# Kernel tuning notes

Hardware: AMD Instinct MI355X
Metric: run time of the kernel (lower is better)

Reference implementation:

```python
import jax, jax.numpy as jnp
import numpy as np

N_NODES = 100000
N_EDGES = 1600000
D_IN = 128
HIDDEN = 64
N_CLASSES = 10
N_GRAPHS = 512


def setup_inputs() -> dict:
    key = jax.random.key(0)
    ks = jax.random.split(key, 9)
    x = jax.random.normal(ks[0], (N_NODES, D_IN), dtype=jnp.float32)
    edge_index = jax.random.randint(ks[1], (2, N_EDGES), 0, N_NODES, dtype=jnp.int32)
    batch = jnp.sort(jax.random.randint(ks[2], (N_NODES,), 0, N_GRAPHS, dtype=jnp.int32))
    # GCNConv: lin (no bias) + separate bias added after aggregation
    s1 = 1.0 / np.sqrt(D_IN)
    s2 = 1.0 / np.sqrt(HIDDEN)
    W1 = jax.random.uniform(ks[3], (D_IN, HIDDEN), jnp.float32, -s1, s1)
    b1 = jnp.zeros((HIDDEN,), jnp.float32)
    W2 = jax.random.uniform(ks[4], (HIDDEN, HIDDEN), jnp.float32, -s2, s2)
    b2 = jnp.zeros((HIDDEN,), jnp.float32)
    Wfc = jax.random.uniform(ks[5], (HIDDEN, N_CLASSES), jnp.float32, -s2, s2)
    bfc = jax.random.uniform(ks[6], (N_CLASSES,), jnp.float32, -s2, s2)
    return {"x": x, "edge_index": edge_index, "batch": batch,
            "W1": W1, "b1": b1, "W2": W2, "b2": b2, "Wfc": Wfc, "bfc": bfc}


def gcn_conv(x, src, dst, W, b, n_nodes):
    # symmetric normalization with added self-loops (PyG gcn_norm defaults)
    deg = jnp.zeros((n_nodes,), x.dtype).at[dst].add(1.0) + 1.0  # +1 self-loop
    dinv = jax.lax.rsqrt(deg)
    h = x @ W  # [N, out]
    coef = (dinv[src] * dinv[dst])[:, None]          # [E, 1]
    msg = h[src] * coef                               # [E, out]
    agg = jax.ops.segment_sum(msg, dst, num_segments=n_nodes)
    agg = agg + h * (dinv * dinv)[:, None]            # self-loop contribution
    return agg + b


def reference(x, edge_index, batch, W1, b1, W2, b2, Wfc, bfc):
    src, dst = edge_index[0], edge_index[1]
    n_nodes = x.shape[0]
    h = gcn_conv(x, src, dst, W1, b1, n_nodes)
    h = jax.nn.relu(h)
    # dropout skipped (inference, training=False)
    h = gcn_conv(h, src, dst, W2, b2, n_nodes)
    h = jax.nn.relu(h)
    # global mean pool over graphs
    sums = jax.ops.segment_sum(h, batch, num_segments=N_GRAPHS)
    cnts = jax.ops.segment_sum(jnp.ones((n_nodes,), h.dtype), batch, num_segments=N_GRAPHS)
    pooled = sums / jnp.maximum(cnts, 1.0)[:, None]   # [G, hidden]
    logits = pooled @ Wfc + bfc                        # [G, classes]
    return jax.nn.log_softmax(logits, axis=1)
```

## Files before the change

### kernel.cpp

```cpp
#include <hip/hip_runtime.h>
#include <cstdint>
#include <cstddef>

#define N_NODES   100000
#define N_EDGES   1600000
#define D_IN      128
#define HIDDEN    64
#define N_GRAPHS  512
#define N_CLASSES 10

#define NB   196
#define EB   1563
#define EB4  391
#define NBE  (NB * EB)
#define BCAP 12288
#define PSLOTS 8

typedef __attribute__((ext_vector_type(8))) short bf16x8;
typedef __attribute__((ext_vector_type(4))) float f32x4;
typedef __attribute__((ext_vector_type(2))) float f32x2;

__device__ inline float bf2f(unsigned short u) {
    return __uint_as_float(((unsigned int)u) << 16);
}
__device__ inline unsigned short f2bf(float f) {
    unsigned int x = __float_as_uint(f);
    return (unsigned short)((x + 0x7FFF + ((x >> 16) & 1)) >> 16);
}

__global__ __launch_bounds__(256)
void scan1_kernel(const int* __restrict__ in, int* __restrict__ bsum, int n) {
    __shared__ int lds[256];
    int tid = threadIdx.x;
    int base = blockIdx.x * 4096 + tid * 16;
    int s = 0;
#pragma unroll
    for (int j = 0; j < 16; j++) { int i = base + j; if (i < n) s += in[i]; }
    lds[tid] = s; __syncthreads();
    for (int off = 128; off > 0; off >>= 1) {
        if (tid < off) lds[tid] += lds[tid + off];
        __syncthreads();
    }
    if (tid == 0) bsum[blockIdx.x] = lds[0];
}

__global__ __launch_bounds__(256)
void scan2_kernel(int* __restrict__ bsum, int* __restrict__ out, int nb, int n) {
    __shared__ int lds[256];
    int tid = threadIdx.x;
    int v = (tid < nb) ? bsum[tid] : 0;
    lds[tid] = v; __syncthreads();
    for (int off = 1; off < 256; off <<= 1) {
        int t = (tid >= off) ? lds[tid - off] : 0;
        __syncthreads();
        lds[tid] += t;
        __syncthreads();
    }
    if (tid < nb) bsum[tid] = lds[tid] - v;
    if (tid == 255) out[n] = lds[255];
}

__global__ __launch_bounds__(256)
void scan3_kernel(const int* __restrict__ in, const int* __restrict__ bsum,
                  int* __restrict__ out, int n) {
    __shared__ int lds[256];
    int tid = threadIdx.x;
    int base = blockIdx.x * 4096 + tid * 16;
    int v[16]; int s = 0;
#pragma unroll
    for (int j = 0; j < 16; j++) {
        int i = base + j;
        v[j] = (i < n) ? in[i] : 0;
        s += v[j];
    }
    lds[tid] = s; __syncthreads();
    for (int off = 1; off < 256; off <<= 1) {
        int t = (tid >= off) ? lds[tid - off] : 0;
        __syncthreads();
        lds[tid] += t;
        __syncthreads();
    }
    int ex = lds[tid] - s + bsum[blockIdx.x];
#pragma unroll
    for (int j = 0; j < 16; j++) {
        int i = base + j;
        if (i < n) { out[i] = ex; ex += v[j]; }
    }
}

__global__ __launch_bounds__(256)
void fused1_kernel(const float* __restrict__ X, const float* __restrict__ W,
                   unsigned short* __restrict__ H,
                   const int* __restrict__ dst, int* __restrict__ HA) {
    const int tid = threadIdx.x;
    if (blockIdx.x & 1) {
        __shared__ int cnt[NB];
        int hb = blockIdx.x >> 1;
        for (int i = tid; i < NB; i += 256) cnt[i] = 0;
        __syncthreads();
        int base = hb * 1024 + tid;
#pragma unroll
        for (int j = 0; j < 4; j++) {
            int t = base + j * 256;
            if (t < N_EDGES) atomicAdd(&cnt[dst[t] >> 9], 1);
        }
        __syncthreads();
        for (int b = tid; b < NB; b += 256) HA[b * EB + hb] = cnt[b];
        return;
    }

    constexpr int K  = D_IN;
    constexpr int KP = K + 8;
    __shared__ unsigned short As[64 * KP];
    __shared__ unsigned short Wt[64 * KP];

    const int row0 = (blockIdx.x >> 1) * 64;

    for (int i = tid; i < K * 64; i += 256) {
        int k = i >> 6;
        int n = i & 63;
        Wt[n * KP + k] = f2bf(W[i]);
    }
    constexpr int KQ = K / 4;
    for (int i = tid; i < 64 * KQ; i += 256) {
        int r = i / KQ, k4 = i % KQ;
        int row = row0 + r;
        float4 v = make_float4(0.f, 0.f, 0.f, 0.f);
        if (row < N_NODES) v = ((const float4*)(X + (size_t)row * K))[k4];
        ushort4 o = make_ushort4(f2bf(v.x), f2bf(v.y), f2bf(v.z), f2bf(v.w));
        *(ushort4*)&As[r * KP + k4 * 4] = o;
    }
    __syncthreads();

    const int wave = tid >> 6;
    const int lane = tid & 63;
    const int lrow = lane & 15;
    const int quad = lane >> 4;
    const int m = wave * 16 + lrow;

    f32x4 acc0 = {0.f, 0.f, 0.f, 0.f};
    f32x4 acc1 = {0.f, 0.f, 0.f, 0.f};
    f32x4 acc2 = {0.f, 0.f, 0.f, 0.f};
    f32x4 acc3 = {0.f, 0.f, 0.f, 0.f};

#pragma unroll
    for (int kt = 0; kt < K / 32; kt++) {
        int k0 = kt * 32 + quad * 8;
        bf16x8 a = *(const bf16x8*)&As[m * KP + k0];
        bf16x8 b0 = *(const bf16x8*)&Wt[(0 * 16 + lrow) * KP + k0];
        bf16x8 b1 = *(const bf16x8*)&Wt[(1 * 16 + lrow) * KP + k0];
        bf16x8 b2 = *(const bf16x8*)&Wt[(2 * 16 + lrow) * KP + k0];
        bf16x8 b3 = *(const bf16x8*)&Wt[(3 * 16 + lrow) * KP + k0];
        acc0 = __builtin_amdgcn_mfma_f32_16x16x32_bf16(a, b0, acc0, 0, 0, 0);
        acc1 = __builtin_amdgcn_mfma_f32_16x16x32_bf16(a, b1, acc1, 0, 0, 0);
        acc2 = __builtin_amdgcn_mfma_f32_16x16x32_bf16(a, b2, acc2, 0, 0, 0);
        acc3 = __builtin_amdgcn_mfma_f32_16x16x32_bf16(a, b3, acc3, 0, 0, 0);
    }

    f32x4 accs[4] = {acc0, acc1, acc2, acc3};
#pragma unroll
    for (int c = 0; c < 4; c++) {
#pragma unroll
        for (int r = 0; r < 4; r++) {
            int row = row0 + wave * 16 + quad * 4 + r;
            if (row < N_NODES) H[(size_t)row * 64 + c * 16 + lrow] = f2bf(accs[c][r]);
        }
    }
}

__global__ __launch_bounds__(256)
void scatterA2_kernel(const int* __restrict__ src, const int* __restrict__ dst,
                      const int* __restrict__ posA, int2* __restrict__ edgeA) {
    __shared__ int off[NB];
    int tid = threadIdx.x, blk = blockIdx.x;
    for (int b = tid; b < NB; b += 256) off[b] = posA[b * EB + blk * 4];
    __syncthreads();
    int base = blk * 4096 + tid;
#pragma unroll
    for (int j = 0; j < 16; j++) {
        int t = base + j * 256;
        if (t < N_EDGES) {
            int d = dst[t];
            int r = atomicAdd(&off[d >> 9], 1);
            edgeA[r] = make_int2(d, src[t]);
        }
    }
}

__global__ __launch_bounds__(256)
void passB_kernel(const int* __restrict__ posA, const int2* __restrict__ edgeA,
                  int* __restrict__ noffs, float* __restrict__ dinv,
                  int* __restrict__ srcs2, unsigned short* __restrict__ hbuf) {
    __shared__ int hist[512];
    __shared__ int off[512];
    __shared__ int ps[256];
    __shared__ int srcs_l[BCAP];

    int tid = threadIdx.x, b = blockIdx.x;
    int e0 = posA[b * EB];
    int e1 = posA[(b + 1) * EB];
    int n0 = b << 9;
    int nn = min(512, N_NODES - n0);
    int len = e1 - e0;

    hist[tid] = 0; hist[tid + 256] = 0;
    __syncthreads();
    for (int i = e0 + tid; i < e1; i += 256) atomicAdd(&hist[edgeA[i].x - n0], 1);
    __syncthreads();

    for (int n = tid; n < nn; n += 256) dinv[n0 + n] = rsqrtf((float)hist[n] + 1.0f);

    int a0 = hist[2 * tid], a1 = hist[2 * tid + 1];
    ps[tid] = a0 + a1;
    __syncthreads();
    for (int d = 1; d < 256; d <<= 1) {
        int v = (tid >= d) ? ps[tid - d] : 0;
        __syncthreads();
        ps[tid] += v;
        __syncthreads();
    }
    int pre = ps[tid] - (a0 + a1);
    off[2 * tid] = pre;
    off[2 * tid + 1] = pre + a0;
    __syncthreads();

    for (int n = tid; n < nn; n += 256) noffs[n0 + n] = e0 + off[n];
    if (b == NB - 1 && tid == 0) noffs[N_NODES] = N_EDGES;
    __syncthreads();

    if (len <= BCAP) {
        for (int i = e0 + tid; i < e1; i += 256) {
            int2 e = edgeA[i];
            int r = atomicAdd(&off[e.x - n0], 1);
            srcs_l[r] = e.y;
        }
        __syncthreads();
        for (int i = tid; i < len; i += 256) srcs2[e0 + i] = srcs_l[i];
    } else {
        for (int i = e0 + tid; i < e1; i += 256) {
            int2 e = edgeA[i];
            int r = atomicAdd(&off[e.x - n0], 1);
            srcs2[e0 + r] = e.y;
        }
    }

    for (int idx = tid; idx < nn * 8; idx += 256) {
        int n  = idx >> 3;
        int c8 = (idx & 7) * 8;
        float d = rsqrtf((float)hist[n] + 1.0f);
        unsigned short* p = hbuf + (size_t)(n0 + n) * 64 + c8;
        int4 u = *(const int4*)p;
        int4 o;
        {
            unsigned int a = (unsigned int)u.x;
            unsigned short l = f2bf(__uint_as_float(a << 16) * d);
            unsigned short h = f2bf(__uint_as_float(a & 0xFFFF0000u) * d);
            o.x = (int)((unsigned int)l | ((unsigned int)h << 16));
        }
        {
            unsigned int a = (unsigned int)u.y;
            unsigned short l = f2bf(__uint_as_float(a << 16) * d);
            unsigned short h = f2bf(__uint_as_float(a & 0xFFFF0000u) * d);
            o.y = (int)((unsigned int)l | ((unsigned int)h << 16));
        }
        {
            unsigned int a = (unsigned int)u.z;
            unsigned short l = f2bf(__uint_as_float(a << 16) * d);
            unsigned short h = f2bf(__uint_as_float(a & 0xFFFF0000u) * d);
            o.z = (int)((unsigned int)l | ((unsigned int)h << 16));
        }
        {
            unsigned int a = (unsigned int)u.w;
            unsigned short l = f2bf(__uint_as_float(a << 16) * d);
            unsigned short h = f2bf(__uint_as_float(a & 0xFFFF0000u) * d);
            o.w = (int)((unsigned int)l | ((unsigned int)h << 16));
        }
        *(int4*)p = o;
    }
}

__device__ inline void upk_add(int4 u, float* acc) {
    unsigned int a = (unsigned int)u.x, b = (unsigned int)u.y;
    unsigned int d = (unsigned int)u.z, e = (unsigned int)u.w;
    acc[0] += __uint_as_float(a << 16);
    acc[1] += __uint_as_float(a & 0xFFFF0000u);
    acc[2] += __uint_as_float(b << 16);
    acc[3] += __uint_as_float(b & 0xFFFF0000u);
    acc[4] += __uint_as_float(d << 16);
    acc[5] += __uint_as_float(d & 0xFFFF0000u);
    acc[6] += __uint_as_float(e << 16);
    acc[7] += __uint_as_float(e & 0xFFFF0000u);
}

__device__ inline void upk8_add(int2 u, float* acc) {
    f32x2 p0 = __builtin_amdgcn_cvt_pk_f32_fp8(u.x, false);
    f32x2 p1 = __builtin_amdgcn_cvt_pk_f32_fp8(u.x, true);
    f32x2 p2 = __builtin_amdgcn_cvt_pk_f32_fp8(u.y, false);
    f32x2 p3 = __builtin_amdgcn_cvt_pk_f32_fp8(u.y, true);
    acc[0] += p0.x; acc[1] += p0.y;
    acc[2] += p1.x; acc[3] += p1.y;
    acc[4] += p2.x; acc[5] += p2.y;
    acc[6] += p3.x; acc[7] += p3.y;
}

__global__ __launch_bounds__(512)
void gather1_gemm2_kernel(const int* __restrict__ offs, const int* __restrict__ srcs,
                          const float* __restrict__ dinv, const unsigned short* __restrict__ h,
                          const float* __restrict__ b1v, const float* __restrict__ W2,
                          unsigned char* __restrict__ H8, int n_nodes) {
    constexpr int KP = 72;
    __shared__ unsigned short Hs[64 * KP];
    __shared__ unsigned short Wt[64 * KP];

    const int tid   = threadIdx.x;
    const int node0 = blockIdx.x * 64;

    for (int i = tid; i < 64 * 64; i += 512) {
        int k = i >> 6;
        int n = i & 63;
        Wt[n * KP + k] = f2bf(W2[i]);
    }

    const int g    = tid >> 3;
    const int node = node0 + g;
    const int cg   = (tid & 7) * 8;

    float acc[8];
#pragma unroll
    for (int j = 0; j < 8; j++) acc[j] = 0.f;
    float dn = 0.f;

    if (node < n_nodes) {
        dn = dinv[node];
        int4 us = *(const int4*)(h + (size_t)node * 64 + cg);
        upk_add(us, acc);

        int i = offs[node];
        const int i1 = offs[node + 1];
        int rem = i1 - i;
        if (rem > 0) {
            int s[8];
#pragma unroll
            for (int j = 0; j < 8; j++) s[j] = srcs[i + (j < rem ? j : rem - 1)];
            while (rem > 0) {
                int4 u8[8];
#pragma unroll
                for (int j = 0; j < 8; j++)
                    u8[j] = *(const int4*)(h + (size_t)s[j] * 64 + cg);
                const int cur  = rem < 8 ? rem : 8;
                const int ni   = i + cur;
                const int nrem = rem - cur;
                if (nrem > 0) {
#pragma unroll
                    for (int j = 0; j < 8; j++)
                        s[j] = srcs[ni + (j < nrem ? j : nrem - 1)];
                }
#pragma unroll
                for (int j = 0; j < 8; j++) { if (j < cur) upk_add(u8[j], acc); }
                i = ni; rem = nrem;
            }
        }
    }

    {
        float4 bv0 = *(const float4*)(b1v + cg);
        float4 bv1 = *(const float4*)(b1v + cg + 4);
        float r0 = fmaxf(dn * acc[0] + bv0.x, 0.f);
        float r1 = fmaxf(dn * acc[1] + bv0.y, 0.f);
        float r2 = fmaxf(dn * acc[2] + bv0.z, 0.f);
        float r3 = fmaxf(dn * acc[3] + bv0.w, 0.f);
        float r4 = fmaxf(dn * acc[4] + bv1.x, 0.f);
        float r5 = fmaxf(dn * acc[5] + bv1.y, 0.f);
        float r6 = fmaxf(dn * acc[6] + bv1.z, 0.f);
        float r7 = fmaxf(dn * acc[7] + bv1.w, 0.f);
        ushort4 p0 = make_ushort4(f2bf(r0), f2bf(r1), f2bf(r2), f2bf(r3));
        ushort4 p1 = make_ushort4(f2bf(r4), f2bf(r5), f2bf(r6), f2bf(r7));
        *(ushort4*)&Hs[g * KP + cg]     = p0;
        *(ushort4*)&Hs[g * KP + cg + 4] = p1;
    }
    __syncthreads();

    const int wave = tid >> 6;
    const int lane = tid & 63;
    const int lrow = lane & 15;
    const int quad = lane >> 4;
    const int rt = (wave & 3) * 16;
    const int ct = (wave >> 2) * 32;
    const int m = rt + lrow;

    f32x4 acc0 = {0.f, 0.f, 0.f, 0.f};
    f32x4 acc1 = {0.f, 0.f, 0.f, 0.f};
#pragma unroll
    for (int kt = 0; kt < 2; kt++) {
        int k0 = kt * 32 + quad * 8;
        bf16x8 a  = *(const bf16x8*)&Hs[m * KP + k0];
        bf16x8 w0 = *(const bf16x8*)&Wt[(ct + lrow) * KP + k0];
        bf16x8 w1 = *(const bf16x8*)&Wt[(ct + 16 + lrow) * KP + k0];
        acc0 = __builtin_amdgcn_mfma_f32_16x16x32_bf16(a, w0, acc0, 0, 0, 0);
        acc1 = __builtin_amdgcn_mfma_f32_16x16x32_bf16(a, w1, acc1, 0, 0, 0);
    }

    f32x4 accs[2] = {acc0, acc1};
#pragma unroll
    for (int r = 0; r < 4; r++) {
        int row = node0 + rt + quad * 4 + r;
        if (row < n_nodes) {
            float dv = dinv[row];
#pragma unroll
            for (int c = 0; c < 2; c++) {
                float v = accs[c][r] * dv;
                int p = __builtin_amdgcn_cvt_pk_fp8_f32(v, v, 0, false);
                H8[(size_t)row * 64 + ct + c * 16 + lrow] = (unsigned char)(p & 0xFF);
            }
        }
    }
}

__global__ __launch_bounds__(256)
void gather_fp8_pool_kernel(const int* __restrict__ offs, const int* __restrict__ srcs,
                            const float* __restrict__ dinv, const unsigned char* __restrict__ h8,
                            const float* __restrict__ b, const int* __restrict__ batch,
                            float* __restrict__ pooled, float* __restrict__ cnt,
                            int n_nodes) {
    __shared__ float pacc[PSLOTS][64];
    __shared__ float lcnt[PSLOTS];
    __shared__ int sg[2];

    int tid = threadIdx.x;
    int node0 = blockIdx.x * 32;
    int lastn = min(node0 + 31, n_nodes - 1);
    for (int i = tid; i < PSLOTS * 64; i += 256) ((float*)pacc)[i] = 0.f;
    if (tid < PSLOTS) lcnt[tid] = 0.f;
    if (tid == 0) { sg[0] = batch[min(node0, n_nodes - 1)]; sg[1] = batch[lastn]; }
    __syncthreads();
    int g0 = sg[0];
    bool single = (sg[0] == sg[1]);

    int node = node0 + (tid >> 3);
    int cg = (tid & 7) * 8;

    float r[8];
#pragma unroll
    for (int j = 0; j < 8; j++) r[j] = 0.f;

    if (node < n_nodes) {
        float dn = dinv[node];
        float acc[8];
#pragma unroll
        for (int j = 0; j < 8; j++) acc[j] = 0.f;
        {
            int2 u = *(const int2*)(h8 + (size_t)node * 64 + cg);
            upk8_add(u, acc);
        }

        int i = offs[node];
        const int i1 = offs[node + 1];
        int rem = i1 - i;
        if (rem > 0) {
            int s[8];
#pragma unroll
            for (int j = 0; j < 8; j++) s[j] = srcs[i + (j < rem ? j : rem - 1)];
            while (rem > 0) {
                int2 u8[8];
#pragma unroll
                for (int j = 0; j < 8; j++)
                    u8[j] = *(const int2*)(h8 + (size_t)s[j] * 64 + cg);
                const int cur  = rem < 8 ? rem : 8;
                const int ni   = i + cur;
                const int nrem = rem - cur;
                if (nrem > 0) {
#pragma unroll
                    for (int j = 0; j < 8; j++)
                        s[j] = srcs[ni + (j < nrem ? j : nrem - 1)];
                }
#pragma unroll
                for (int j = 0; j < 8; j++) { if (j < cur) upk8_add(u8[j], acc); }
                i = ni; rem = nrem;
            }
        }

        float4 b0 = *(const float4*)(b + cg);
        float4 b1 = *(const float4*)(b + cg + 4);
        r[0] = fmaxf(dn * acc[0] + b0.x, 0.f);
        r[1] = fmaxf(dn * acc[1] + b0.y, 0.f);
        r[2] = fmaxf(dn * acc[2] + b0.z, 0.f);
        r[3] = fmaxf(dn * acc[3] + b0.w, 0.f);
        r[4] = fmaxf(dn * acc[4] + b1.x, 0.f);
        r[5] = fmaxf(dn * acc[5] + b1.y, 0.f);
        r[6] = fmaxf(dn * acc[6] + b1.z, 0.f);
        r[7] = fmaxf(dn * acc[7] + b1.w, 0.f);
    }

    if (single) {
#pragma unroll
        for (int j = 0; j < 8; j++) {
            float v = r[j];
            v += __shfl_xor(v, 8);
            v += __shfl_xor(v, 16);
            v += __shfl_xor(v, 32);
            r[j] = v;
        }
        int wave = tid >> 6;
        int lane = tid & 63;
        if (lane < 8) {
#pragma unroll
            for (int j = 0; j < 8; j++) pacc[wave][lane * 8 + j] = r[j];
        }
        __syncthreads();
        if (tid < 64) {
            float s = pacc[0][tid] + pacc[1][tid] + pacc[2][tid] + pacc[3][tid];
            if (s != 0.f) unsafeAtomicAdd(&pooled[(size_t)g0 * 64 + tid], s);
        }
        if (tid == 0) {
            int valid = min(32, n_nodes - node0);
            unsafeAtomicAdd(&cnt[g0], (float)valid);
        }
    } else {
        if (node < n_nodes) {
            int g = batch[node];
            int slot = g - g0;
            if (slot < PSLOTS) {
#pragma unroll
                for (int j = 0; j < 8; j++) atomicAdd(&pacc[slot][cg + j], r[j]);
                if ((tid & 7) == 0) atomicAdd(&lcnt[slot], 1.f);
            } else {
#pragma unroll
                for (int j = 0; j < 8; j++) unsafeAtomicAdd(&pooled[(size_t)g * 64 + cg + j], r[j]);
                if ((tid & 7) == 0) unsafeAtomicAdd(&cnt[g], 1.f);
            }
        }
        __syncthreads();
        for (int i = tid; i < PSLOTS * 64; i += 256) {
            float v = ((float*)pacc)[i];
            if (v != 0.f) unsafeAtomicAdd(&pooled[(size_t)(g0 + (i >> 6)) * 64 + (i & 63)], v);
        }
        if (tid < PSLOTS && lcnt[tid] != 0.f) unsafeAtomicAdd(&cnt[g0 + tid], lcnt[tid]);
    }
}

__global__ __launch_bounds__(256)
void head_kernel(const float* __restrict__ pooled, const float* __restrict__ cnt,
                 const float* __restrict__ Wfc, const float* __restrict__ bfc,
                 float* __restrict__ out) {
    __shared__ float Ws[HIDDEN * N_CLASSES];
    __shared__ float bs[N_CLASSES];
    int tid = threadIdx.x;
    for (int i = tid; i < HIDDEN * N_CLASSES; i += 256) Ws[i] = Wfc[i];
    if (tid < N_CLASSES) bs[tid] = bfc[tid];
    __syncthreads();

    int g = blockIdx.x * 256 + tid;
    if (g >= N_GRAPHS) return;

    float inv = 1.f / fmaxf(cnt[g], 1.f);
    float p[HIDDEN];
#pragma unroll
    for (int k = 0; k < HIDDEN; k++) p[k] = pooled[(size_t)g * 64 + k] * inv;

    float lg[N_CLASSES];
    float m = -1e30f;
#pragma unroll
    for (int j = 0; j < N_CLASSES; j++) {
        float a = bs[j];
#pragma unroll
        for (int k = 0; k < HIDDEN; k++) a += p[k] * Ws[k * N_CLASSES + j];
        lg[j] = a;
        m = fmaxf(m, a);
    }
    float s = 0.f;
#pragma unroll
    for (int j = 0; j < N_CLASSES; j++) s += __expf(lg[j] - m);
    float lse = m + __logf(s);
#pragma unroll
    for (int j = 0; j < N_CLASSES; j++) out[(size_t)g * N_CLASSES + j] = lg[j] - lse;
}

extern "C" void kernel_launch(void* const* d_in, const int* in_sizes, int n_in,
                              void* d_out, int out_size, void* d_ws, size_t ws_size,
                              hipStream_t stream) {
    const float* x   = (const float*)d_in[0];
    const int*   ei  = (const int*)d_in[1];
    const int*   bat = (const int*)d_in[2];
    const float* W1  = (const float*)d_in[3];
    const float* b1  = (const float*)d_in[4];
    const float* W2  = (const float*)d_in[5];
    const float* b2  = (const float*)d_in[6];
    const float* Wfc = (const float*)d_in[7];
    const float* bfc = (const float*)d_in[8];
    float* out = (float*)d_out;

    const int* src = ei;
    const int* dst = ei + N_EDGES;

    char* ws = (char*)d_ws;

    const size_t OFF_H     = 0;
    const size_t OFF_SRCS2 = 12800000;
    const size_t OFF_NOFFS = 19200000;
    const size_t OFF_DINV  = 19600016;
    const size_t OFF_BUFB  = 25600000;
    const size_t OFF_EDGEA = 38400000;
    const size_t OFF_HA    = 51200000;
    const size_t OFF_POSA  = 52425392;
    const size_t OFF_BSUM  = 53650800;
    const size_t OFF_POOL  = 53651824;
    const size_t OFF_CNT   = 53782896;

    unsigned short* hbuf  = (unsigned short*)(ws + OFF_H);
    int*   srcs2  = (int*)  (ws + OFF_SRCS2);
    int*   noffs  = (int*)  (ws + OFF_NOFFS);
    float* dinv   = (float*)(ws + OFF_DINV);
    unsigned char* hbuf8 = (unsigned char*)(ws + OFF_BUFB);
    int2*  edgeA  = (int2*) (ws + OFF_EDGEA);
    int*   HA     = (int*)  (ws + OFF_HA);
    int*   posA   = (int*)  (ws + OFF_POSA);
    int*   bsum   = (int*)  (ws + OFF_BSUM);
    float* pooled = (float*)(ws + OFF_POOL);
    float* cnt    = (float*)(ws + OFF_CNT);

    const int SCAN_BLOCKS = (NBE + 4095) / 4096;
    const int GATHER_BLOCKS = (N_NODES * 8 + 255) / 256;
    const int GEMM_BLOCKS = (N_NODES + 63) / 64;

    hipMemsetAsync(pooled, 0, (size_t)(N_GRAPHS * 64 + N_GRAPHS) * sizeof(float), stream);

    fused1_kernel<<<2 * GEMM_BLOCKS, 256, 0, stream>>>(x, W1, hbuf, dst, HA);
    scan1_kernel<<<SCAN_BLOCKS, 256, 0, stream>>>(HA, bsum, NBE);
    scan2_kernel<<<1, 256, 0, stream>>>(bsum, posA, SCAN_BLOCKS, NBE);
    scan3_kernel<<<SCAN_BLOCKS, 256, 0, stream>>>(HA, bsum, posA, NBE);
    scatterA2_kernel<<<EB4, 256, 0, stream>>>(src, dst, posA, edgeA);
    passB_kernel<<<NB, 256, 0, stream>>>(posA, edgeA, noffs, dinv, srcs2, hbuf);

    gather1_gemm2_kernel<<<GEMM_BLOCKS, 512, 0, stream>>>(
        noffs, srcs2, dinv, hbuf, b1, W2, hbuf8, N_NODES);
    gather_fp8_pool_kernel<<<GATHER_BLOCKS, 256, 0, stream>>>(
        noffs, srcs2, dinv, hbuf8, b2, bat, pooled, cnt, N_NODES);

    head_kernel<<<(N_GRAPHS + 255) / 256, 256, 0, stream>>>(pooled, cnt, Wfc, bfc, out);
}
```

Baseline: 250.1 us.

## Split GEMM1 from histogram, fold dinv scaling into GEMM epilogue, pack edges

Splits the fused histogram/GEMM1 kernel into a standalone histogram kernel and moves GEMM1 after passB. That lets GEMM1 scale its output rows by dinv directly, which removes passB's separate read-modify-write pass over the H buffer. Edge records in the intermediate buffer are packed into one 32-bit word (local dst in the upper bits, src in the lower 17 bits) instead of int2, which halves that traffic. GEMM1 now loads X straight into registers without an LDS staging step. The cost is that the histogram can no longer overlap with the GEMM, and the packing assumes node ids fit in 17 bits.

```diff
diff --git a/kernel.cpp b/kernel.cpp
--- a/kernel.cpp
+++ b/kernel.cpp
@@ -89,54 +89,139 @@
 }
 
 __global__ __launch_bounds__(256)
-void fused1_kernel(const float* __restrict__ X, const float* __restrict__ W,
-                   unsigned short* __restrict__ H,
-                   const int* __restrict__ dst, int* __restrict__ HA) {
+void hist_kernel(const int* __restrict__ dst, int* __restrict__ HA) {
+    __shared__ int cnt[NB];
     const int tid = threadIdx.x;
-    if (blockIdx.x & 1) {
-        __shared__ int cnt[NB];
-        int hb = blockIdx.x >> 1;
-        for (int i = tid; i < NB; i += 256) cnt[i] = 0;
-        __syncthreads();
-        int base = hb * 1024 + tid;
-#pragma unroll
-        for (int j = 0; j < 4; j++) {
-            int t = base + j * 256;
-            if (t < N_EDGES) atomicAdd(&cnt[dst[t] >> 9], 1);
-        }
-        __syncthreads();
-        for (int b = tid; b < NB; b += 256) HA[b * EB + hb] = cnt[b];
-        return;
-    }
-
+    const int hb = blockIdx.x;
+    for (int i = tid; i < NB; i += 256) cnt[i] = 0;
+    __syncthreads();
+    int base = hb * 1024 + tid;
+#pragma unroll
+    for (int j = 0; j < 4; j++) {
+        int t = base + j * 256;
+        if (t < N_EDGES) atomicAdd(&cnt[dst[t] >> 9], 1);
+    }
+    __syncthreads();
+    for (int b = tid; b < NB; b += 256) HA[b * EB + hb] = cnt[b];
+}
+
+__global__ __launch_bounds__(256)
+void scatterA2_kernel(const int* __restrict__ src, const int* __restrict__ dst,
+                      const int* __restrict__ posA, unsigned int* __restrict__ edgeA) {
+    __shared__ int off[NB];
+    int tid = threadIdx.x, blk = blockIdx.x;
+    for (int b = tid; b < NB; b += 256) off[b] = posA[b * EB + blk * 4];
+    __syncthreads();
+    int base = blk * 4096 + tid;
+#pragma unroll
+    for (int j = 0; j < 16; j++) {
+        int t = base + j * 256;
+        if (t < N_EDGES) {
+            int d = dst[t];
+            unsigned int pk = (((unsigned int)(d & 511)) << 17) | (unsigned int)src[t];
+            int r = atomicAdd(&off[d >> 9], 1);
+            edgeA[r] = pk;
+        }
+    }
+}
+
+__global__ __launch_bounds__(256)
+void passB_kernel(const int* __restrict__ posA, const unsigned int* __restrict__ edgeA,
+                  int* __restrict__ noffs, float* __restrict__ dinv,
+                  int* __restrict__ srcs2) {
+    __shared__ int hist[512];
+    __shared__ int off[512];
+    __shared__ int ps[256];
+    __shared__ int srcs_l[BCAP];
+
+    int tid = threadIdx.x, b = blockIdx.x;
+    int e0 = posA[b * EB];
+    int e1 = posA[(b + 1) * EB];
+    int n0 = b << 9;
+    int nn = min(512, N_NODES - n0);
+    int len = e1 - e0;
+
+    hist[tid] = 0; hist[tid + 256] = 0;
+    __syncthreads();
+    for (int i = e0 + tid; i < e1; i += 256) atomicAdd(&hist[edgeA[i] >> 17], 1);
+    __syncthreads();
+
+    for (int n = tid; n < nn; n += 256) dinv[n0 + n] = rsqrtf((float)hist[n] + 1.0f);
+
+    int a0 = hist[2 * tid], a1 = hist[2 * tid + 1];
+    ps[tid] = a0 + a1;
+    __syncthreads();
+    for (int d = 1; d < 256; d <<= 1) {
+        int v = (tid >= d) ? ps[tid - d] : 0;
+        __syncthreads();
+        ps[tid] += v;
+        __syncthreads();
+    }
+    int pre = ps[tid] - (a0 + a1);
+    off[2 * tid] = pre;
+    off[2 * tid + 1] = pre + a0;
+    __syncthreads();
+
+    for (int n = tid; n < nn; n += 256) noffs[n0 + n] = e0 + off[n];
+    if (b == NB - 1 && tid == 0) noffs[N_NODES] = N_EDGES;
+    __syncthreads();
+
+    if (len <= BCAP) {
+        for (int i = e0 + tid; i < e1; i += 256) {
+            unsigned int e = edgeA[i];
+            int r = atomicAdd(&off[e >> 17], 1);
+            srcs_l[r] = (int)(e & 0x1FFFFu);
+        }
+        __syncthreads();
+        for (int i = tid; i < len; i += 256) srcs2[e0 + i] = srcs_l[i];
+    } else {
+        for (int i = e0 + tid; i < e1; i += 256) {
+            unsigned int e = edgeA[i];
+            int r = atomicAdd(&off[e >> 17], 1);
+            srcs2[e0 + r] = (int)(e & 0x1FFFFu);
+        }
+    }
+}
+
+__global__ __launch_bounds__(512)
+void gemm1_kernel(const float* __restrict__ X, const float* __restrict__ W,
+                  const float* __restrict__ dinv, unsigned short* __restrict__ H,
+                  int n_rows) {
     constexpr int K  = D_IN;
     constexpr int KP = K + 8;
-    __shared__ unsigned short As[64 * KP];
     __shared__ unsigned short Wt[64 * KP];
 
-    const int row0 = (blockIdx.x >> 1) * 64;
-
-    for (int i = tid; i < K * 64; i += 256) {
+    const int tid  = threadIdx.x;
+    const int row0 = blockIdx.x * 128;
+
+    for (int i = tid; i < K * 64; i += 512) {
         int k = i >> 6;
         int n = i & 63;
         Wt[n * KP + k] = f2bf(W[i]);
     }
-    constexpr int KQ = K / 4;
-    for (int i = tid; i < 64 * KQ; i += 256) {
-        int r = i / KQ, k4 = i % KQ;
-        int row = row0 + r;
-        float4 v = make_float4(0.f, 0.f, 0.f, 0.f);
-        if (row < N_NODES) v = ((const float4*)(X + (size_t)row * K))[k4];
-        ushort4 o = make_ushort4(f2bf(v.x), f2bf(v.y), f2bf(v.z), f2bf(v.w));
-        *(ushort4*)&As[r * KP + k4 * 4] = o;
-    }
-    __syncthreads();
 
     const int wave = tid >> 6;
     const int lane = tid & 63;
     const int lrow = lane & 15;
     const int quad = lane >> 4;
     const int m = wave * 16 + lrow;
+    const int row = row0 + m;
+    const bool valid = row < n_rows;
+
+    float4 xa[8];
+    if (valid) {
+        const float4* xr4 = (const float4*)(X + (size_t)row * K);
+#pragma unroll
+        for (int kt = 0; kt < 4; kt++) {
+            int q = (kt * 32 + quad * 8) >> 2;
+            xa[2 * kt]     = xr4[q];
+            xa[2 * kt + 1] = xr4[q + 1];
+        }
+    } else {
+#pragma unroll
+        for (int j = 0; j < 8; j++) xa[j] = make_float4(0.f, 0.f, 0.f, 0.f);
+    }
+    __syncthreads();
 
     f32x4 acc0 = {0.f, 0.f, 0.f, 0.f};
     f32x4 acc1 = {0.f, 0.f, 0.f, 0.f};
@@ -144,9 +229,12 @@
     f32x4 acc3 = {0.f, 0.f, 0.f, 0.f};
 
 #pragma unroll
-    for (int kt = 0; kt < K / 32; kt++) {
+    for (int kt = 0; kt < 4; kt++) {
         int k0 = kt * 32 + quad * 8;
-        bf16x8 a = *(const bf16x8*)&As[m * KP + k0];
+        const float* f = (const float*)&xa[2 * kt];
+        bf16x8 a;
+#pragma unroll
+        for (int j = 0; j < 8; j++) a[j] = (short)f2bf(f[j]);
         bf16x8 b0 = *(const bf16x8*)&Wt[(0 * 16 + lrow) * KP + k0];
         bf16x8 b1 = *(const bf16x8*)&Wt[(1 * 16 + lrow) * KP + k0];
         bf16x8 b2 = *(const bf16x8*)&Wt[(2 * 16 + lrow) * KP + k0];
@@ -159,123 +247,14 @@
 
     f32x4 accs[4] = {acc0, acc1, acc2, acc3};
 #pragma unroll
-    for (int c = 0; c < 4; c++) {
-#pragma unroll
-        for (int r = 0; r < 4; r++) {
-            int row = row0 + wave * 16 + quad * 4 + r;
-            if (row < N_NODES) H[(size_t)row * 64 + c * 16 + lrow] = f2bf(accs[c][r]);
-        }
-    }
-}
-
-__global__ __launch_bounds__(256)
-void scatterA2_kernel(const int* __restrict__ src, const int* __restrict__ dst,
-                      const int* __restrict__ posA, int2* __restrict__ edgeA) {
-    __shared__ int off[NB];
-    int tid = threadIdx.x, blk = blockIdx.x;
-    for (int b = tid; b < NB; b += 256) off[b] = posA[b * EB + blk * 4];
-    __syncthreads();
-    int base = blk * 4096 + tid;
-#pragma unroll
-    for (int j = 0; j < 16; j++) {
-        int t = base + j * 256;
-        if (t < N_EDGES) {
-            int d = dst[t];
-            int r = atomicAdd(&off[d >> 9], 1);
-            edgeA[r] = make_int2(d, src[t]);
-        }
-    }
-}
-
-__global__ __launch_bounds__(256)
-void passB_kernel(const int* __restrict__ posA, const int2* __restrict__ edgeA,
-                  int* __restrict__ noffs, float* __restrict__ dinv,
-                  int* __restrict__ srcs2, unsigned short* __restrict__ hbuf) {
-    __shared__ int hist[512];
-    __shared__ int off[512];
-    __shared__ int ps[256];
-    __shared__ int srcs_l[BCAP];
-
-    int tid = threadIdx.x, b = blockIdx.x;
-    int e0 = posA[b * EB];
-    int e1 = posA[(b + 1) * EB];
-    int n0 = b << 9;
-    int nn = min(512, N_NODES - n0);
-    int len = e1 - e0;
-
-    hist[tid] = 0; hist[tid + 256] = 0;
-    __syncthreads();
-    for (int i = e0 + tid; i < e1; i += 256) atomicAdd(&hist[edgeA[i].x - n0], 1);
-    __syncthreads();
-
-    for (int n = tid; n < nn; n += 256) dinv[n0 + n] = rsqrtf((float)hist[n] + 1.0f);
-
-    int a0 = hist[2 * tid], a1 = hist[2 * tid + 1];
-    ps[tid] = a0 + a1;
-    __syncthreads();
-    for (int d = 1; d < 256; d <<= 1) {
-        int v = (tid >= d) ? ps[tid - d] : 0;
-        __syncthreads();
-        ps[tid] += v;
-        __syncthreads();
-    }
-    int pre = ps[tid] - (a0 + a1);
-    off[2 * tid] = pre;
-    off[2 * tid + 1] = pre + a0;
-    __syncthreads();
-
-    for (int n = tid; n < nn; n += 256) noffs[n0 + n] = e0 + off[n];
-    if (b == NB - 1 && tid == 0) noffs[N_NODES] = N_EDGES;
-    __syncthreads();
-
-    if (len <= BCAP) {
-        for (int i = e0 + tid; i < e1; i += 256) {
-            int2 e = edgeA[i];
-            int r = atomicAdd(&off[e.x - n0], 1);
-            srcs_l[r] = e.y;
-        }
-        __syncthreads();
-        for (int i = tid; i < len; i += 256) srcs2[e0 + i] = srcs_l[i];
-    } else {
-        for (int i = e0 + tid; i < e1; i += 256) {
-            int2 e = edgeA[i];
-            int r = atomicAdd(&off[e.x - n0], 1);
-            srcs2[e0 + r] = e.y;
-        }
-    }
-
-    for (int idx = tid; idx < nn * 8; idx += 256) {
-        int n  = idx >> 3;
-        int c8 = (idx & 7) * 8;
-        float d = rsqrtf((float)hist[n] + 1.0f);
-        unsigned short* p = hbuf + (size_t)(n0 + n) * 64 + c8;
-        int4 u = *(const int4*)p;
-        int4 o;
-        {
-            unsigned int a = (unsigned int)u.x;
-            unsigned short l = f2bf(__uint_as_float(a << 16) * d);
-            unsigned short h = f2bf(__uint_as_float(a & 0xFFFF0000u) * d);
-            o.x = (int)((unsigned int)l | ((unsigned int)h << 16));
-        }
-        {
-            unsigned int a = (unsigned int)u.y;
-            unsigned short l = f2bf(__uint_as_float(a << 16) * d);
-            unsigned short h = f2bf(__uint_as_float(a & 0xFFFF0000u) * d);
-            o.y = (int)((unsigned int)l | ((unsigned int)h << 16));
-        }
-        {
-            unsigned int a = (unsigned int)u.z;
-            unsigned short l = f2bf(__uint_as_float(a << 16) * d);
-            unsigned short h = f2bf(__uint_as_float(a & 0xFFFF0000u) * d);
-            o.z = (int)((unsigned int)l | ((unsigned int)h << 16));
-        }
-        {
-            unsigned int a = (unsigned int)u.w;
-            unsigned short l = f2bf(__uint_as_float(a << 16) * d);
-            unsigned short h = f2bf(__uint_as_float(a & 0xFFFF0000u) * d);
-            o.w = (int)((unsigned int)l | ((unsigned int)h << 16));
-        }
-        *(int4*)p = o;
+    for (int r = 0; r < 4; r++) {
+        int orow = row0 + wave * 16 + quad * 4 + r;
+        if (orow < n_rows) {
+            float dv = dinv[orow];
+#pragma unroll
+            for (int c = 0; c < 4; c++)
+                H[(size_t)orow * 64 + c * 16 + lrow] = f2bf(accs[c][r] * dv);
+        }
     }
 }
 
@@ -611,7 +590,7 @@
     int*   noffs  = (int*)  (ws + OFF_NOFFS);
     float* dinv   = (float*)(ws + OFF_DINV);
     unsigned char* hbuf8 = (unsigned char*)(ws + OFF_BUFB);
-    int2*  edgeA  = (int2*) (ws + OFF_EDGEA);
+    unsigned int* edgeA = (unsigned int*)(ws + OFF_EDGEA);
     int*   HA     = (int*)  (ws + OFF_HA);
     int*   posA   = (int*)  (ws + OFF_POSA);
     int*   bsum   = (int*)  (ws + OFF_BSUM);
@@ -620,18 +599,19 @@
 
     const int SCAN_BLOCKS = (NBE + 4095) / 4096;
     const int GATHER_BLOCKS = (N_NODES * 8 + 255) / 256;
-    const int GEMM_BLOCKS = (N_NODES + 63) / 64;
+    const int GEMM2_BLOCKS = (N_NODES + 63) / 64;
+    const int GEMM1_BLOCKS = (N_NODES + 127) / 128;
 
     hipMemsetAsync(pooled, 0, (size_t)(N_GRAPHS * 64 + N_GRAPHS) * sizeof(float), stream);
 
-    fused1_kernel<<<2 * GEMM_BLOCKS, 256, 0, stream>>>(x, W1, hbuf, dst, HA);
+    hist_kernel<<<EB, 256, 0, stream>>>(dst, HA);
     scan1_kernel<<<SCAN_BLOCKS, 256, 0, stream>>>(HA, bsum, NBE);
     scan2_kernel<<<1, 256, 0, stream>>>(bsum, posA, SCAN_BLOCKS, NBE);
     scan3_kernel<<<SCAN_BLOCKS, 256, 0, stream>>>(HA, bsum, posA, NBE);
     scatterA2_kernel<<<EB4, 256, 0, stream>>>(src, dst, posA, edgeA);
-    passB_kernel<<<NB, 256, 0, stream>>>(posA, edgeA, noffs, dinv, srcs2, hbuf);
-
-    gather1_gemm2_kernel<<<GEMM_BLOCKS, 512, 0, stream>>>(
+    passB_kernel<<<NB, 256, 0, stream>>>(posA, edgeA, noffs, dinv, srcs2);
+    gemm1_kernel<<<GEMM1_BLOCKS, 512, 0, stream>>>(x, W1, dinv, hbuf, N_NODES);
+    gather1_gemm2_kernel<<<GEMM2_BLOCKS, 512, 0, stream>>>(
         noffs, srcs2, dinv, hbuf, b1, W2, hbuf8, N_NODES);
     gather_fp8_pool_kernel<<<GATHER_BLOCKS, 256, 0, stream>>>(
         noffs, srcs2, dinv, hbuf8, b2, bat, pooled, cnt, N_NODES);
```

Result: faster. 230.3 us (-7.9%).
